# Kernel tuning notes

Hardware: AMD Instinct MI355X
Metric: run time of the kernel (lower is better)

Reference implementation:

```python
import jax, jax.numpy as jnp
import numpy as np
import math

B = 1024
INPUT_SHAPE = (8, 8, 8, 8)
OUTPUT_SHAPE = (8, 8, 8, 8)
RANK_SHAPE = (2, 2, 2, 2)
BLOCK_NUM = 4
OUTPUT_SIZE = int(np.prod(OUTPUT_SHAPE))
CORE_SIZE = int(np.prod(RANK_SHAPE))


def setup_inputs() -> dict:
    key = jax.random.key(0)
    k1, k2, k3 = jax.random.split(key, 3)
    stdv = 1.0 / math.sqrt(OUTPUT_SIZE)  # reset_parameters: uniform(-stdv, stdv)
    inputs = jax.random.normal(k1, (B, int(np.prod(INPUT_SHAPE))), dtype=jnp.float32)
    # core_block{b}: shape rank_shape; factor{j}_block{b}: shape (I_j, O_j, R_j)
    cores = jax.random.uniform(k2, (BLOCK_NUM,) + RANK_SHAPE, minval=-stdv, maxval=stdv, dtype=jnp.float32)
    factors = jax.random.uniform(
        k3, (BLOCK_NUM, len(RANK_SHAPE), INPUT_SHAPE[0], OUTPUT_SHAPE[0], RANK_SHAPE[0]),
        minval=-stdv, maxval=stdv, dtype=jnp.float32)
    return {"inputs": inputs, "cores": cores, "factors": factors}


def reference(inputs, cores, factors):
    Bn = inputs.shape[0]
    # view(-1, *input_shape) then permute(0, n, n-1, ..., 1)
    x = inputs.reshape(Bn, *INPUT_SHAPE)
    x = jnp.transpose(x, (0, 4, 3, 2, 1))  # [B, i3, i2, i1, i0]
    res = jnp.zeros((Bn, OUTPUT_SIZE), dtype=inputs.dtype)
    for b in range(BLOCK_NUM):
        cal = x
        factor_offset = 1
        for j in range(len(RANK_SHAPE)):
            f = factors[b, j]            # (I, J, R)
            I, J, R = f.shape
            cal = cal.reshape(-1, I) @ f.reshape(I, J * R)
            cal = cal.reshape(Bn * factor_offset, -1, J * R)
            cal = jnp.transpose(cal, (0, 2, 1))
            factor_offset *= J
        # contract with core flattened row-major (exactly as core.view(core_size, -1))
        cal = cal.reshape(-1, CORE_SIZE) @ cores[b].reshape(CORE_SIZE, 1)
        res = res + cal.reshape(Bn, -1)
    return res
```

## Files before the change

### kernel.cpp

```cpp
#include <hip/hip_runtime.h>
#include <hip/hip_bf16.h>
#include <stdint.h>

typedef __attribute__((ext_vector_type(8))) __bf16 bf16x8;
typedef __attribute__((ext_vector_type(4))) float f32x4;
typedef __attribute__((ext_vector_type(8))) unsigned short u16x8;

__device__ __forceinline__ unsigned short f2bf(float f) {
    unsigned u = __builtin_bit_cast(unsigned, f);
    return (unsigned short)((u + 0x7fffu + ((u >> 16) & 1u)) >> 16);
}

__device__ __forceinline__ void glds16(const void* g, void* l) {
    __builtin_amdgcn_global_load_lds(
        (const __attribute__((address_space(1))) unsigned int*)(uintptr_t)g,
        (__attribute__((address_space(3))) unsigned int*)l, 16, 0, 0);
}

#define VMCNT(n) asm volatile("s_waitcnt vmcnt(" #n ")" ::: "memory")
#define BAR()                                  \
    do {                                       \
        asm volatile("" ::: "memory");         \
        __builtin_amdgcn_s_barrier();          \
        asm volatile("" ::: "memory");         \
    } while (0)

__global__ __launch_bounds__(256) void prep_slabs(const float* __restrict__ factors,
                                                  const float* __restrict__ cores,
                                                  unsigned short* __restrict__ Aslab,
                                                  unsigned short* __restrict__ Bslab) {
    int idx = blockIdx.x * 256 + threadIdx.x;
    int e = idx & 65535;
    int grp = e >> 12;
    int m = (e >> 4) & 255;
    int k = e & 15;
    int b = k >> 2, q = k & 3, r0 = q >> 1, r1 = q & 1;
    int base = (e >> 4) * 32;
    if (idx < 65536) {
        int o01 = grp * 4 + (m >> 6), a01 = m & 63;
        int o0 = o01 >> 3, o1 = o01 & 7, a0 = a01 >> 3, a1 = a01 & 7;
        float v = factors[b*512 +   0 + a0*16 + o0*2 + r0]
                * factors[b*512 + 128 + a1*16 + o1*2 + r1];
        Aslab[base + k] = f2bf(v);
        Aslab[base + k + 16] = 0;
    } else {
        int o23 = grp * 4 + (m >> 6), a23 = m & 63;
        int o2 = o23 >> 3, o3 = o23 & 7, a2 = a23 >> 3, a3 = a23 & 7;
        float s = 0.f;
#pragma unroll
        for (int r2 = 0; r2 < 2; ++r2)
#pragma unroll
            for (int r3 = 0; r3 < 2; ++r3)
                s += factors[b*512 + 256 + a2*16 + o2*2 + r2]
                   * factors[b*512 + 384 + a3*16 + o3*2 + r3]
                   * cores[b*16 + r3*8 + r2*4 + r1*2 + r0];
        Bslab[base + k] = f2bf(s);
        Bslab[base + k + 16] = 0;
    }
}

__global__ __launch_bounds__(256) void cvt_bf16(const float4* __restrict__ in,
                                                ushort4* __restrict__ out) {
    int i = blockIdx.x * 256 + threadIdx.x;
    float4 v = in[i];
    ushort4 o;
    o.x = f2bf(v.x); o.y = f2bf(v.y); o.z = f2bf(v.z); o.w = f2bf(v.w);
    out[i] = o;
}

__global__ __launch_bounds__(256) void build_w2(const unsigned short* __restrict__ Aslab,
                                                const unsigned short* __restrict__ Bslab,
                                                unsigned short* __restrict__ Wt) {
    __shared__ unsigned short As2[256 * 40];
    __shared__ unsigned short Bs2[256 * 40];
    __shared__ unsigned short lbuf[4 * 64 * 72];
    const int tid = threadIdx.x, lane = tid & 63, w = tid >> 6;
    const int bo = blockIdx.x >> 4, bn4 = blockIdx.x & 15;

    const u16x8* srcA = (const u16x8*)(Aslab + ((size_t)bo * 256 + tid) * 32);
    const u16x8* srcB = (const u16x8*)(Bslab + ((size_t)bn4 * 256 + tid) * 32);
#pragma unroll
    for (int i = 0; i < 4; ++i) {
        *(u16x8*)&As2[tid * 40 + i * 8] = srcA[i];
        *(u16x8*)&Bs2[tid * 40 + i * 8] = srcB[i];
    }
    __syncthreads();

    const int fr = lane & 15, fh = lane >> 4;
    bf16x8 af[4];
#pragma unroll
    for (int mf = 0; mf < 4; ++mf)
        af[mf] = *(const bf16x8*)&As2[(w * 64 + mf * 16 + fr) * 40 + fh * 8];

    for (int wn = 0; wn < 4; ++wn) {
        f32x4 acc[4][4] = {};
        bf16x8 bf_[4];
#pragma unroll
        for (int nf = 0; nf < 4; ++nf)
            bf_[nf] = *(const bf16x8*)&Bs2[(wn * 64 + nf * 16 + fr) * 40 + fh * 8];
#pragma unroll
        for (int mf = 0; mf < 4; ++mf)
#pragma unroll
            for (int nf = 0; nf < 4; ++nf)
                acc[mf][nf] = __builtin_amdgcn_mfma_f32_16x16x32_bf16(
                    af[mf], bf_[nf], acc[mf][nf], 0, 0, 0);
#pragma unroll
        for (int mf = 0; mf < 4; ++mf)
#pragma unroll
            for (int nf = 0; nf < 4; ++nf)
#pragma unroll
                for (int j = 0; j < 4; ++j)
                    lbuf[w * 4608 + (mf * 16 + fh * 4 + j) * 72 + nf * 16 + fr] =
                        f2bf(acc[mf][nf][j]);
        const int o = (bo * 4 + w) * 64 + bn4 * 4 + wn;
        unsigned short* dst = Wt + (size_t)o * 4096;
#pragma unroll
        for (int i = 0; i < 8; ++i) {
            int c = i * 64 + lane;
            *(u16x8*)&dst[c * 8] =
                *(const u16x8*)&lbuf[w * 4608 + (c >> 3) * 72 + (c & 7) * 8];
        }
    }
}

__global__ __launch_bounds__(256, 2) void gemm_bt64(const unsigned short* __restrict__ A,
                                                    const unsigned short* __restrict__ Bt,
                                                    float* __restrict__ C) {
    constexpr int K = 4096;
    constexpr int N = 4096;
    constexpr int BK = 64;
    constexpr int NT = K / BK;
    __shared__ alignas(16) char lds[3][24576];
    const int tid = threadIdx.x;
    const int lane = tid & 63, w = tid >> 6;
    const int wm = w >> 1, wn = w & 1;
    const int xcd = blockIdx.x & 7, r = blockIdx.x >> 3;
    const int bn = xcd * 4 + (r & 3);
    const int bm = r >> 2;

    const unsigned short* gA[2]; const unsigned short* gB[4];
    int lAoff[2], lBoff[4];
#pragma unroll
    for (int i = 0; i < 2; ++i) {
        int cs = i * 256 + tid;
        int row = cs >> 3;
        int c = (cs & 7) ^ ((row >> 1) & 7);
        gA[i] = A + (size_t)(bm * 64 + row) * K + c * 8;
        lAoff[i] = i * 4096 + w * 1024;
    }
#pragma unroll
    for (int i = 0; i < 4; ++i) {
        int cs = i * 256 + tid;
        int row = cs >> 3;
        int c = (cs & 7) ^ ((row >> 1) & 7);
        gB[i] = Bt + (size_t)(bn * 128 + row) * K + c * 8;
        lBoff[i] = 8192 + i * 4096 + w * 1024;
    }

#define STAGE(buf, kt)                                                        \
    do {                                                                      \
        _Pragma("unroll")                                                     \
        for (int i = 0; i < 2; ++i) glds16(gA[i] + (kt), &lds[buf][lAoff[i]]);\
        _Pragma("unroll")                                                     \
        for (int i = 0; i < 4; ++i) glds16(gB[i] + (kt), &lds[buf][lBoff[i]]);\
    } while (0)

    const int fr = lane & 15, fh = lane >> 4;
    const int sk = (fr >> 1) & 7;
    int aoff[2], boff[2];
#pragma unroll
    for (int kk = 0; kk < 2; ++kk) {
        aoff[kk] = (wm * 32 + fr) * 128 + (((kk * 4 + fh) ^ sk) << 4);
        boff[kk] = 8192 + (wn * 64 + fr) * 128 + (((kk * 4 + fh) ^ sk) << 4);
    }

    f32x4 acc[2][4] = {};

#define COMPUTE(buf)                                                          \
    do {                                                                      \
        const char* base = &lds[buf][0];                                      \
        _Pragma("unroll")                                                     \
        for (int kk = 0; kk < 2; ++kk) {                                      \
            bf16x8 af2[2], bf4[4];                                            \
            _Pragma("unroll")                                                 \
            for (int m = 0; m < 2; ++m)                                       \
                af2[m] = *(const bf16x8*)(base + aoff[kk] + m * 2048);        \
            _Pragma("unroll")                                                 \
            for (int n = 0; n < 4; ++n)                                       \
                bf4[n] = *(const bf16x8*)(base + boff[kk] + n * 2048);        \
            _Pragma("unroll")                                                 \
            for (int m = 0; m < 2; ++m)                                       \
                _Pragma("unroll")                                             \
                for (int n = 0; n < 4; ++n)                                   \
                    acc[m][n] = __builtin_amdgcn_mfma_f32_16x16x32_bf16(      \
                        af2[m], bf4[n], acc[m][n], 0, 0, 0);                  \
        }                                                                     \
    } while (0)

#define PHASE(tb, sbuf, cbuf)                                                 \
    do {                                                                      \
        STAGE(sbuf, ((tb) + 2) * BK);                                         \
        VMCNT(12);                                                            \
        BAR();                                                                \
        COMPUTE(cbuf);                                                        \
        BAR();                                                                \
    } while (0)

    STAGE(0, 0);
    STAGE(1, BK);
    for (int t = 0; t < 60; t += 3) {
        PHASE(t, 2, 0);
        PHASE(t + 1, 0, 1);
        PHASE(t + 2, 1, 2);
    }
    PHASE(60, 2, 0);
    PHASE(61, 0, 1);
    VMCNT(6);  BAR(); COMPUTE(2); BAR();
    VMCNT(0);  BAR(); COMPUTE(0);

    const int crow0 = bm * 64 + wm * 32 + fh * 4;
    const int ccol0 = bn * 128 + wn * 64 + fr;
#pragma unroll
    for (int m = 0; m < 2; ++m)
#pragma unroll
        for (int n = 0; n < 4; ++n)
#pragma unroll
            for (int j = 0; j < 4; ++j)
                C[(size_t)(crow0 + m * 16 + j) * N + (ccol0 + n * 16)] = acc[m][n][j];
#undef STAGE
#undef COMPUTE
#undef PHASE
}

extern "C" void kernel_launch(void* const* d_in, const int* in_sizes, int n_in,
                              void* d_out, int out_size, void* d_ws, size_t ws_size,
                              hipStream_t stream) {
    const float* inputs  = (const float*)d_in[0];
    const float* cores   = (const float*)d_in[1];
    const float* factors = (const float*)d_in[2];
    float* out = (float*)d_out;

    char* ws = (char*)d_ws;
    unsigned short* xb    = (unsigned short*)ws;
    unsigned short* Wt    = (unsigned short*)(ws + (8u << 20));
    unsigned short* Aslab = (unsigned short*)(ws + (40u << 20));
    unsigned short* Bslab = Aslab + 131072;

    prep_slabs<<<512, 256, 0, stream>>>(factors, cores, Aslab, Bslab);
    cvt_bf16<<<4096, 256, 0, stream>>>((const float4*)inputs, (ushort4*)xb);
    build_w2<<<256, 256, 0, stream>>>(Aslab, Bslab, Wt);
    gemm_bt64<<<512, 256, 0, stream>>>(xb, Wt, out);
}
```

Measured before the change: 64.11 us.

## Fuse slab prep, bf16 conversion and weight build into one kernel

The prep_slabs, cvt_bf16 and build_w2 launches are merged into a single prep_fused kernel. Extra blocks at the top of the grid do the input bf16 conversion. The other blocks compute their A and B factor slabs directly into LDS, so the global slab round trip is gone. The weight-build work is also split 4x finer, one wn tile per block, to raise parallelism, at the cost of recomputing the A slab in every block and launching 1024 build blocks instead of 256.

```diff
diff --git a/kernel.cpp b/kernel.cpp
--- a/kernel.cpp
+++ b/kernel.cpp
@@ -25,101 +25,89 @@
         asm volatile("" ::: "memory");         \
     } while (0)
 
-__global__ __launch_bounds__(256) void prep_slabs(const float* __restrict__ factors,
+__global__ __launch_bounds__(256) void prep_fused(const float* __restrict__ factors,
                                                   const float* __restrict__ cores,
-                                                  unsigned short* __restrict__ Aslab,
-                                                  unsigned short* __restrict__ Bslab) {
-    int idx = blockIdx.x * 256 + threadIdx.x;
-    int e = idx & 65535;
-    int grp = e >> 12;
-    int m = (e >> 4) & 255;
-    int k = e & 15;
-    int b = k >> 2, q = k & 3, r0 = q >> 1, r1 = q & 1;
-    int base = (e >> 4) * 32;
-    if (idx < 65536) {
-        int o01 = grp * 4 + (m >> 6), a01 = m & 63;
-        int o0 = o01 >> 3, o1 = o01 & 7, a0 = a01 >> 3, a1 = a01 & 7;
-        float v = factors[b*512 +   0 + a0*16 + o0*2 + r0]
-                * factors[b*512 + 128 + a1*16 + o1*2 + r1];
-        Aslab[base + k] = f2bf(v);
-        Aslab[base + k + 16] = 0;
-    } else {
-        int o23 = grp * 4 + (m >> 6), a23 = m & 63;
-        int o2 = o23 >> 3, o3 = o23 & 7, a2 = a23 >> 3, a3 = a23 & 7;
-        float s = 0.f;
-#pragma unroll
-        for (int r2 = 0; r2 < 2; ++r2)
-#pragma unroll
-            for (int r3 = 0; r3 < 2; ++r3)
-                s += factors[b*512 + 256 + a2*16 + o2*2 + r2]
-                   * factors[b*512 + 384 + a3*16 + o3*2 + r3]
-                   * cores[b*16 + r3*8 + r2*4 + r1*2 + r0];
-        Bslab[base + k] = f2bf(s);
-        Bslab[base + k + 16] = 0;
-    }
-}
-
-__global__ __launch_bounds__(256) void cvt_bf16(const float4* __restrict__ in,
-                                                ushort4* __restrict__ out) {
-    int i = blockIdx.x * 256 + threadIdx.x;
-    float4 v = in[i];
-    ushort4 o;
-    o.x = f2bf(v.x); o.y = f2bf(v.y); o.z = f2bf(v.z); o.w = f2bf(v.w);
-    out[i] = o;
-}
-
-__global__ __launch_bounds__(256) void build_w2(const unsigned short* __restrict__ Aslab,
-                                                const unsigned short* __restrict__ Bslab,
-                                                unsigned short* __restrict__ Wt) {
+                                                  const float4* __restrict__ xin,
+                                                  ushort4* __restrict__ xb,
+                                                  unsigned short* __restrict__ Wt) {
+    if (blockIdx.x >= 1024) {
+        int i = (blockIdx.x - 1024) * 256 + threadIdx.x;
+        float4 v = xin[i];
+        ushort4 o;
+        o.x = f2bf(v.x); o.y = f2bf(v.y); o.z = f2bf(v.z); o.w = f2bf(v.w);
+        xb[i] = o;
+        return;
+    }
     __shared__ unsigned short As2[256 * 40];
-    __shared__ unsigned short Bs2[256 * 40];
+    __shared__ unsigned short Bs2[64 * 40];
     __shared__ unsigned short lbuf[4 * 64 * 72];
     const int tid = threadIdx.x, lane = tid & 63, w = tid >> 6;
-    const int bo = blockIdx.x >> 4, bn4 = blockIdx.x & 15;
-
-    const u16x8* srcA = (const u16x8*)(Aslab + ((size_t)bo * 256 + tid) * 32);
-    const u16x8* srcB = (const u16x8*)(Bslab + ((size_t)bn4 * 256 + tid) * 32);
-#pragma unroll
-    for (int i = 0; i < 4; ++i) {
-        *(u16x8*)&As2[tid * 40 + i * 8] = srcA[i];
-        *(u16x8*)&Bs2[tid * 40 + i * 8] = srcB[i];
+    const int bo = blockIdx.x >> 6, bn4 = (blockIdx.x >> 2) & 15, wn = blockIdx.x & 3;
+
+    {
+        int o01 = bo * 4 + (tid >> 6), a01 = tid & 63;
+        int o0 = o01 >> 3, o1 = o01 & 7, a0 = a01 >> 3, a1 = a01 & 7;
+#pragma unroll
+        for (int k = 0; k < 16; ++k) {
+            int b = k >> 2, q = k & 3, r0 = q >> 1, r1 = q & 1;
+            float v = factors[b*512 +   0 + a0*16 + o0*2 + r0]
+                    * factors[b*512 + 128 + a1*16 + o1*2 + r1];
+            As2[tid * 40 + k] = f2bf(v);
+            As2[tid * 40 + 16 + k] = 0;
+        }
+    }
+    {
+        int o23 = bn4 * 4 + wn, o2 = o23 >> 3, o3 = o23 & 7;
+#pragma unroll
+        for (int rep = 0; rep < 4; ++rep) {
+            int task = rep * 256 + tid;
+            int n = task >> 4, k = task & 15;
+            int a2 = n >> 3, a3 = n & 7;
+            int b = k >> 2, q = k & 3, r0 = q >> 1, r1 = q & 1;
+            float s = 0.f;
+#pragma unroll
+            for (int r2 = 0; r2 < 2; ++r2)
+#pragma unroll
+                for (int r3 = 0; r3 < 2; ++r3)
+                    s += factors[b*512 + 256 + a2*16 + o2*2 + r2]
+                       * factors[b*512 + 384 + a3*16 + o3*2 + r3]
+                       * cores[b*16 + r3*8 + r2*4 + r1*2 + r0];
+            Bs2[n * 40 + k] = f2bf(s);
+            Bs2[n * 40 + 16 + k] = 0;
+        }
     }
     __syncthreads();
 
     const int fr = lane & 15, fh = lane >> 4;
-    bf16x8 af[4];
+    bf16x8 af[4], bf_[4];
 #pragma unroll
     for (int mf = 0; mf < 4; ++mf)
         af[mf] = *(const bf16x8*)&As2[(w * 64 + mf * 16 + fr) * 40 + fh * 8];
-
-    for (int wn = 0; wn < 4; ++wn) {
-        f32x4 acc[4][4] = {};
-        bf16x8 bf_[4];
+#pragma unroll
+    for (int nf = 0; nf < 4; ++nf)
+        bf_[nf] = *(const bf16x8*)&Bs2[(nf * 16 + fr) * 40 + fh * 8];
+    f32x4 acc[4][4] = {};
+#pragma unroll
+    for (int mf = 0; mf < 4; ++mf)
 #pragma unroll
         for (int nf = 0; nf < 4; ++nf)
-            bf_[nf] = *(const bf16x8*)&Bs2[(wn * 64 + nf * 16 + fr) * 40 + fh * 8];
-#pragma unroll
-        for (int mf = 0; mf < 4; ++mf)
-#pragma unroll
-            for (int nf = 0; nf < 4; ++nf)
-                acc[mf][nf] = __builtin_amdgcn_mfma_f32_16x16x32_bf16(
-                    af[mf], bf_[nf], acc[mf][nf], 0, 0, 0);
-#pragma unroll
-        for (int mf = 0; mf < 4; ++mf)
-#pragma unroll
-            for (int nf = 0; nf < 4; ++nf)
-#pragma unroll
-                for (int j = 0; j < 4; ++j)
-                    lbuf[w * 4608 + (mf * 16 + fh * 4 + j) * 72 + nf * 16 + fr] =
-                        f2bf(acc[mf][nf][j]);
-        const int o = (bo * 4 + w) * 64 + bn4 * 4 + wn;
-        unsigned short* dst = Wt + (size_t)o * 4096;
-#pragma unroll
-        for (int i = 0; i < 8; ++i) {
-            int c = i * 64 + lane;
-            *(u16x8*)&dst[c * 8] =
-                *(const u16x8*)&lbuf[w * 4608 + (c >> 3) * 72 + (c & 7) * 8];
-        }
+            acc[mf][nf] = __builtin_amdgcn_mfma_f32_16x16x32_bf16(
+                af[mf], bf_[nf], acc[mf][nf], 0, 0, 0);
+#pragma unroll
+    for (int mf = 0; mf < 4; ++mf)
+#pragma unroll
+        for (int nf = 0; nf < 4; ++nf)
+#pragma unroll
+            for (int j = 0; j < 4; ++j)
+                lbuf[w * 4608 + (mf * 16 + fh * 4 + j) * 72 + nf * 16 + fr] =
+                    f2bf(acc[mf][nf][j]);
+    const int o = (bo * 4 + w) * 64 + bn4 * 4 + wn;
+    unsigned short* dst = Wt + (size_t)o * 4096;
+#pragma unroll
+    for (int i = 0; i < 8; ++i) {
+        int c = i * 64 + lane;
+        *(u16x8*)&dst[c * 8] =
+            *(const u16x8*)&lbuf[w * 4608 + (c >> 3) * 72 + (c & 7) * 8];
     }
 }
 
@@ -241,13 +229,10 @@
     float* out = (float*)d_out;
 
     char* ws = (char*)d_ws;
-    unsigned short* xb    = (unsigned short*)ws;
-    unsigned short* Wt    = (unsigned short*)(ws + (8u << 20));
-    unsigned short* Aslab = (unsigned short*)(ws + (40u << 20));
-    unsigned short* Bslab = Aslab + 131072;
-
-    prep_slabs<<<512, 256, 0, stream>>>(factors, cores, Aslab, Bslab);
-    cvt_bf16<<<4096, 256, 0, stream>>>((const float4*)inputs, (ushort4*)xb);
-    build_w2<<<256, 256, 0, stream>>>(Aslab, Bslab, Wt);
+    unsigned short* xb = (unsigned short*)ws;
+    unsigned short* Wt = (unsigned short*)(ws + (8u << 20));
+
+    prep_fused<<<5120, 256, 0, stream>>>(factors, cores,
+                                         (const float4*)inputs, (ushort4*)xb, Wt);
     gemm_bt64<<<512, 256, 0, stream>>>(xb, Wt, out);
 }
```

After: 64.44 us. Within noise of the previous version (+0.5%).
